# Kernel optimization log

Hardware: AMD Instinct MI355X
Metric: run time of the kernel (lower is better)

The kernel has to match this reference:

```python
import jax, jax.numpy as jnp
import numpy as np

MAXTIME = 1406073600
MINTIME = 832550400
SPAN = 10000
TIME_EMB = 100
N_GATE = 8
NUM_INTEREST = 4
DIM = 64
SEQ = 256
BATCH = 1024
ALPHA = 0.1
PI = 3.14159  # matches the literal in the source


def _build_time_table():
    # TimeEncoder: interleaved sin/cos positional table over time buckets.
    n = MAXTIME // SPAN + 3
    pos = np.arange(n, dtype=np.float64)[:, None]
    div = np.exp(np.arange(TIME_EMB // 2, dtype=np.float64) * -(np.log(10000.0) / TIME_EMB))[None, :]
    te = np.zeros((n, TIME_EMB), dtype=np.float32)
    te[:, 0::2] = np.sin(pos * div)
    te[:, 1::2] = np.cos(pos * div)
    return jnp.asarray(te)

_TIME_TABLE = _build_time_table()


def _time_encode(t):
    idx = (t / SPAN).astype(jnp.int32)
    return _TIME_TABLE[idx - jnp.min(idx)]


def setup_inputs() -> dict:
    key = jax.random.key(0)
    ks = jax.random.split(key, 11)
    B, S, D, NI, G = BATCH, SEQ, DIM, NUM_INTEREST, N_GATE
    item_his_emb = jax.random.normal(ks[0], (B, S, D), jnp.float32)
    item_eb = jax.random.normal(ks[1], (B, D), jnp.float32)
    # query times near maxtime, history times strictly earlier -> positive deltas
    t_batch = MAXTIME - 1e6 * jax.random.uniform(ks[2], (B,), jnp.float32)
    t_his = MINTIME + (MAXTIME - MINTIME - 1e6) * jax.random.uniform(ks[3], (B, S), jnp.float32)
    mask = (jax.random.uniform(ks[4], (B, S)) > 0.3).astype(jnp.float32)
    W1 = jax.random.normal(ks[5], (3 * TIME_EMB, 100), jnp.float32) / np.sqrt(3 * TIME_EMB)
    b1 = jnp.zeros((100,), jnp.float32)
    W2 = jax.random.normal(ks[6], (100, 1), jnp.float32) * 0.1
    b2 = jnp.zeros((1,), jnp.float32)
    phase = 100000.0 * jax.random.uniform(ks[7], (1, 1, G), jnp.float32)
    tao = 86400.0 * jnp.array([[[1, 2, 7, 14, 30, 60, 365, 730]]], jnp.float32)
    ratio = 0.3 * jax.random.uniform(ks[8], (1, 1, G), jnp.float32)
    gate_emb = jax.random.normal(ks[9], (1, D, G), jnp.float32)
    w_bilinear = jax.random.normal(ks[10], (S, NI * D, D), jnp.float32)
    return {"item_his_emb": item_his_emb, "item_eb": item_eb, "t_batch": t_batch,
            "t_his": t_his, "mask": mask, "W1": W1, "b1": b1, "W2": W2, "b2": b2,
            "phase": phase, "tao": tao, "ratio": ratio, "gate_emb": gate_emb,
            "w_bilinear": w_bilinear, "ta": 2}


def reference(item_his_emb, item_eb, t_batch, t_his, mask, W1, b1, W2, b2,
              phase, tao, ratio, gate_emb, w_bilinear, ta):
    B, S, D = item_his_emb.shape
    NI = NUM_INTEREST
    # --- time factor ---
    t_tiled = jnp.broadcast_to(t_batch[:, None], (B, S))
    time_feature = jnp.concatenate([_time_encode(t_tiled), _time_encode(t_his),
                                    _time_encode(t_tiled - t_his)], axis=2)  # [B,S,300]
    hidden1 = jax.nn.relu(time_feature @ W1 + b1)
    t_factor = jnp.transpose(jax.nn.sigmoid(hidden1 @ W2 + b2), (0, 2, 1))  # [B,1,S]
    # --- circadian gate factor ---
    phi = jnp.mod(t_his[:, :, None] - phase, tao) / tao  # [B,S,G]
    gate = jnp.where(phi < ratio, jnp.maximum(jnp.sin(PI * phi / ratio), 0.0), ALPHA * phi)
    gate_ratio = jax.nn.softmax(jnp.einsum('bsd,dg->bsg', item_his_emb, gate_emb[0]), axis=2) * gate
    g_factor = jnp.sum(gate_ratio, axis=2)[:, None, :]  # [B,1,S]
    reg1 = jnp.linalg.norm(t_factor)
    reg2 = jnp.linalg.norm(ratio) + jnp.linalg.norm(phase) / 100000.0
    # ta == 2 branch
    loss_reg = 0.1 * reg1 + 1.0 * reg2 + 1.0 / reg1 + 0.1 / reg2
    factor = jnp.broadcast_to(t_factor + g_factor, (B, NI, S))
    # --- bilinear_type == 2 projection ---
    item_emb_hat = jnp.einsum('skd,bsd->bsk', w_bilinear, item_his_emb)  # [B,S,NI*D]
    item_emb_hat = item_emb_hat.reshape(B, S, NI, D).transpose(0, 2, 1, 3)  # [B,NI,S,D]
    hat_iter = jax.lax.stop_gradient(item_emb_hat)
    # --- dynamic routing, 3 iterations ---
    cw = jnp.zeros((B, NI, S), item_his_emb.dtype)
    amask = mask[:, None, :]
    cap = None
    for i in range(3):
        sw = jax.nn.softmax(cw, axis=1)           # softmax over interests
        sw = jnp.where(amask == 0, 0.0, sw)
        src = hat_iter if i < 2 else item_emb_hat
        cap = jnp.einsum('bks,bksd->bkd', sw, src)  # [B,NI,D]
        n2 = jnp.sum(cap * cap, axis=-1, keepdims=True)
        cap = (n2 / (1.0 + n2) / jnp.sqrt(n2 + 1e-9)) * cap  # squash
        if i < 2:
            delta = jnp.einsum('bksd,bkd->bks', hat_iter, cap) * factor
            cw = cw + delta
    interest_capsule = cap  # [B,NI,D]
    # --- hard readout ---
    atten = jax.nn.softmax(jnp.einsum('bkd,bd->bk', interest_capsule, item_eb), axis=1)
    readout = interest_capsule[jnp.arange(B), jnp.argmax(atten, axis=1)]  # [B,D]
    return interest_capsule, readout, loss_reg
```

## Files before the change

### kernel.cpp

```cpp
#include <hip/hip_runtime.h>
#include <math.h>
#include <limits.h>

#define BB 1024
#define SS 256
#define DD 64
#define NI 4
#define NG 8
#define TE_N 100
#define PMAX 57420
#define PMAXP 57424
#define P0MAX 128
#define TPB 16

typedef _Float16 half8 __attribute__((ext_vector_type(8)));
typedef _Float16 half4 __attribute__((ext_vector_type(4)));
typedef float f32x4 __attribute__((ext_vector_type(4)));

#define OFF_FTHT  ((size_t)0)
#define OFF_FDFT  ((size_t)TE_N*PMAXP)
#define OFF_GTBP  (OFF_FDFT + (size_t)TE_N*PMAXP)
#define OFF_FAC   (OFF_GTBP + (size_t)TE_N*P0MAX)
#define OFF_SCAL  (OFF_FAC + (size_t)BB*SS)
#define OFF_REC   (OFF_SCAL + 160)
#define OFF_SREC  (OFF_REC + (size_t)BB*SS*2)
#define OFF_HAT   (OFF_SREC + (size_t)BB*SS*2)

__device__ inline float dpp_add_xor1(float x){
    int i = __builtin_bit_cast(int, x);
    int p = __builtin_amdgcn_update_dpp(i, i, 0xB1, 0xF, 0xF, true);
    return x + __builtin_bit_cast(float, p);
}
__device__ inline float dpp_add_xor2(float x){
    int i = __builtin_bit_cast(int, x);
    int p = __builtin_amdgcn_update_dpp(i, i, 0x4E, 0xF, 0xF, true);
    return x + __builtin_bit_cast(float, p);
}
__device__ inline float swz_add_xor16(float x){
    int i = __builtin_bit_cast(int, x);
    int p = __builtin_amdgcn_ds_swizzle(i, 0x401F);
    return x + __builtin_bit_cast(float, p);
}

__global__ void k_init(float* ws){
    int t = threadIdx.x;
    int* ib = (int*)(ws + OFF_SCAL);
    if (t == 0){
        ib[0] = INT_MAX; ib[1] = INT_MAX; ib[2] = INT_MAX;
        ws[OFF_SCAL + 4] = 0.0f;
    }
    if (t >= 8 && t < 136) ib[t] = 0;
}

__global__ void k_min(const float* __restrict__ tb, const float* __restrict__ th, float* ws){
    int gid = blockIdx.x * blockDim.x + threadIdx.x;
    int stride = gridDim.x * blockDim.x;
    int m0 = INT_MAX, m1 = INT_MAX, m2 = INT_MAX;
    for (int i = gid; i < BB*SS; i += stride){
        float t  = th[i];
        float t2 = tb[i >> 8];
        int i1 = (int)(t / 10000.0f);
        int i2 = (int)((t2 - t) / 10000.0f);
        m1 = min(m1, i1);
        m2 = min(m2, i2);
    }
    if (gid < BB) m0 = (int)(tb[gid] / 10000.0f);
    #pragma unroll
    for (int off = 1; off < 64; off <<= 1){
        m0 = min(m0, __shfl_xor(m0, off));
        m1 = min(m1, __shfl_xor(m1, off));
        m2 = min(m2, __shfl_xor(m2, off));
    }
    if ((threadIdx.x & 63) == 0){
        int* mi = (int*)(ws + OFF_SCAL);
        atomicMin(mi + 0, m0);
        atomicMin(mi + 1, m1);
        atomicMin(mi + 2, m2);
    }
}

__global__ void k_tables(const float* __restrict__ W1, float* ws){
    int pbase = blockIdx.x * TPB;
    int t = threadIdx.x;
    __shared__ float te[TPB][TE_N];
    for (int idx = t; idx < TPB*50; idx += 128){
        int pp = idx / 50, h = idx - pp*50;
        double div = exp((double)h * -0.09210340371976184);
        double a = (double)(pbase + pp) * div;
        te[pp][2*h]   = (float)sin(a);
        te[pp][2*h+1] = (float)cos(a);
    }
    __syncthreads();
    if (t < TE_N){
        float a1[TPB], a2[TPB];
        #pragma unroll
        for (int pp = 0; pp < TPB; pp++){ a1[pp] = 0.f; a2[pp] = 0.f; }
        for (int i = 0; i < TE_N; i++){
            float w1v = W1[(100+i)*100 + t];
            float w2v = W1[(200+i)*100 + t];
            #pragma unroll
            for (int pp = 0; pp < TPB; pp++){
                float v = te[pp][i];
                a1[pp] += v * w1v;
                a2[pp] += v * w2v;
            }
        }
        for (int pp = 0; pp < TPB; pp++){
            int p = pbase + pp;
            if (p < PMAX){
                ws[OFF_FTHT + (size_t)t*PMAXP + p] = a1[pp];
                ws[OFF_FDFT + (size_t)t*PMAXP + p] = a2[pp];
            }
        }
    }
}

__global__ void k_gtbP(const float* __restrict__ W1, const float* __restrict__ b1, float* ws){
    int p0 = blockIdx.x;
    int t = threadIdx.x;
    __shared__ float te[TE_N];
    if (t < TE_N/2){
        double div = exp((double)t * -0.09210340371976184);
        double a = (double)p0 * div;
        te[2*t]   = (float)sin(a);
        te[2*t+1] = (float)cos(a);
    }
    __syncthreads();
    if (t < TE_N){
        float a1 = b1[t];
        for (int i = 0; i < TE_N; i++) a1 += te[i] * W1[i*100 + t];
        ws[OFF_GTBP + (size_t)t*P0MAX + p0] = a1;
    }
}

__global__ void __launch_bounds__(256) k_hist(const float* __restrict__ tb,
                                              const float* __restrict__ th, float* ws){
    __shared__ int lh[64];
    int t = threadIdx.x;
    if (t < 64) lh[t] = 0;
    __syncthreads();
    int gid = blockIdx.x*256 + t;
    int b = gid >> 8;
    const int* mi = (const int*)(ws + OFF_SCAL);
    float thv = th[gid], tbv = tb[b];
    int p1 = (int)(thv / 10000.0f) - mi[1];
    int p2 = (int)((tbv - thv) / 10000.0f) - mi[2];
    int p0 = (int)(tbv / 10000.0f) - mi[0];
    p1 = min(max(p1, 0), PMAX-1);
    p2 = min(max(p2, 0), PMAX-1);
    p0 = min(max(p0, 0), P0MAX-1);
    ((uint2*)(ws + OFF_REC))[gid] =
        make_uint2((unsigned)p1 | ((unsigned)p2 << 16), (unsigned)gid | ((unsigned)p0 << 20));
    atomicAdd(&lh[p1 >> 10], 1);
    __syncthreads();
    if (t < 64 && lh[t]) atomicAdd((int*)(ws + OFF_SCAL) + 8 + t, lh[t]);
}

__global__ void k_scan(float* ws){
    if (threadIdx.x == 0){
        int* g   = (int*)(ws + OFF_SCAL) + 8;
        int* cur = (int*)(ws + OFF_SCAL) + 72;
        int acc = 0;
        for (int i = 0; i < 64; i++){ cur[i] = acc; acc += g[i]; }
    }
}

__global__ void __launch_bounds__(256) k_scatter(float* ws){
    __shared__ int lh[64], lbase[64];
    int t = threadIdx.x;
    if (t < 64) lh[t] = 0;
    __syncthreads();
    int gid = blockIdx.x*256 + t;
    uint2 r = ((const uint2*)(ws + OFF_REC))[gid];
    int bkt = (int)(r.x & 0xFFFFu) >> 10;
    int myloc = atomicAdd(&lh[bkt], 1);
    __syncthreads();
    if (t < 64 && lh[t]) lbase[t] = atomicAdd((int*)(ws + OFF_SCAL) + 72 + t, lh[t]);
    __syncthreads();
    ((uint2*)(ws + OFF_SREC))[lbase[bkt] + myloc] = r;
}

__global__ void __launch_bounds__(256) k_factor2(const float* __restrict__ W2,
                         const float* __restrict__ b2, float* ws){
    int t = threadIdx.x;
    int bid = blockIdx.x;
    int sbid = (bid & 7)*128 + (bid >> 3);
    int q = sbid*256 + t;
    uint2 r = ((const uint2*)(ws + OFF_SREC))[q];
    int p1  = (int)(r.x & 0xFFFFu);
    int p2  = (int)(r.x >> 16);
    int gid = (int)(r.y & 0xFFFFFu);
    int p0  = (int)(r.y >> 20);

    const float* ft = ws + OFF_FTHT + p1;
    const float* fd = ws + OFF_FDFT + p2;
    const float* gp = ws + OFF_GTBP + p0;

    float z = 0.f;
    #pragma unroll 10
    for (int j = 0; j < TE_N; j++){
        float a = ft[(size_t)j*PMAXP];
        float c = fd[(size_t)j*PMAXP];
        float g = gp[(size_t)j*P0MAX];
        z += fmaxf(g + a + c, 0.f) * W2[j];
    }
    float tf = 1.f / (1.f + expf(-(z + b2[0])));
    ws[OFF_FAC + gid] = tf;

    float r1 = tf * tf;
    #pragma unroll
    for (int off = 1; off < 64; off <<= 1) r1 += __shfl_xor(r1, off);
    if ((t & 63) == 0) atomicAdd(ws + OFF_SCAL + 4, r1);
}

__global__ void __launch_bounds__(256) k_gate(const float* __restrict__ X,
      const float* __restrict__ th_, const float* __restrict__ phase,
      const float* __restrict__ tao, const float* __restrict__ ratio,
      const float* __restrict__ ge, float* ws){
    __shared__ float sge[NG][DD];
    int t = threadIdx.x;
    for (int i = t; i < DD*NG; i += 256) sge[i & 7][i >> 3] = ge[i];
    __syncthreads();
    int gid = blockIdx.x * 256 + t;

    float lg[NG];
    #pragma unroll
    for (int g = 0; g < NG; g++) lg[g] = 0.f;
    const float4* xr = (const float4*)(X + (size_t)gid*DD);
    #pragma unroll 4
    for (int dc = 0; dc < 16; dc++){
        float4 xv = xr[dc];
        #pragma unroll
        for (int g = 0; g < NG; g++){
            lg[g] += xv.x*sge[g][dc*4+0] + xv.y*sge[g][dc*4+1]
                   + xv.z*sge[g][dc*4+2] + xv.w*sge[g][dc*4+3];
        }
    }
    float mx = lg[0];
    #pragma unroll
    for (int g = 1; g < NG; g++) mx = fmaxf(mx, lg[g]);
    float thv = th_[gid];
    float es = 0.f, gf = 0.f;
    #pragma unroll
    for (int g = 0; g < NG; g++){
        float e = expf(lg[g] - mx);
        es += e;
        float phv = fmodf(thv - phase[g], tao[g]) / tao[g];
        float gv = (phv < ratio[g]) ? fmaxf(sinf(3.14159f*phv/ratio[g]), 0.f) : 0.1f*phv;
        gf += e * gv;
    }
    ws[OFF_FAC + gid] += gf / es;
}

__global__ void __launch_bounds__(512, 2)
k_hat(const float* __restrict__ X, const float* __restrict__ Wb,
      float* __restrict__ hat, int b0, int nb){
    int btile = blockIdx.x;
    int s     = blockIdx.y;
    int t     = threadIdx.x;
    int rows = nb - btile*64; if (rows > 64) rows = 64;

    __shared__ _Float16 lds[40960];

    const float* xbase = X + ((size_t)(b0 + btile*64)*SS + s)*DD;
    #pragma unroll
    for (int i = 0; i < 2; i++){
        int q = t + 512*i;
        int r = q >> 4, jf = q & 15;
        float4 v;
        if (r < rows) v = *(const float4*)(xbase + (size_t)r*SS*DD + jf*4);
        else { v.x = 0.f; v.y = 0.f; v.z = 0.f; v.w = 0.f; }
        half4 h, l;
        h.x = (_Float16)v.x; h.y = (_Float16)v.y; h.z = (_Float16)v.z; h.w = (_Float16)v.w;
        l.x = (_Float16)(v.x - (float)h.x); l.y = (_Float16)(v.y - (float)h.y);
        l.z = (_Float16)(v.z - (float)h.z); l.w = (_Float16)(v.w - (float)h.w);
        int bt = r >> 4, rowin = r & 15;
        int j0 = jf*4;
        int kk = j0 >> 5, jb = (j0 & 31) >> 3, e0 = j0 & 7;
        int lane = rowin + 16*jb;
        int base = ((bt*2 + kk)*2)*512 + lane*8 + e0;
        *(half4*)(lds + base)       = h;
        *(half4*)(lds + base + 512) = l;
    }
    const float* wbase = Wb + (size_t)s*16384;
    #pragma unroll
    for (int i = 0; i < 8; i++){
        int q = t + 512*i;
        int kd = q >> 4, jf = q & 15;
        float4 v = *(const float4*)(wbase + kd*64 + jf*4);
        half4 h, l;
        h.x = (_Float16)v.x; h.y = (_Float16)v.y; h.z = (_Float16)v.z; h.w = (_Float16)v.w;
        l.x = (_Float16)(v.x - (float)h.x); l.y = (_Float16)(v.y - (float)h.y);
        l.z = (_Float16)(v.z - (float)h.z); l.w = (_Float16)(v.w - (float)h.w);
        int kdt = kd >> 4, rowin = kd & 15;
        int j0 = jf*4;
        int kk = j0 >> 5, jb = (j0 & 31) >> 3, e0 = j0 & 7;
        int lane = rowin + 16*jb;
        int base = 8192 + ((kdt*2 + kk)*2)*512 + lane*8 + e0;
        *(half4*)(lds + base)       = h;
        *(half4*)(lds + base + 512) = l;
    }
    __syncthreads();

    int w    = t >> 6;
    int lane = t & 63;
    int wbt  = w >> 1;
    int kdh  = w & 1;

    half8 a[2][2];
    #pragma unroll
    for (int kk = 0; kk < 2; kk++)
        #pragma unroll
        for (int hl = 0; hl < 2; hl++)
            a[kk][hl] = *(half8*)(lds + ((wbt*2 + kk)*2 + hl)*512 + lane*8);

    int brow = (lane >> 4) * 4;
    int bcol = lane & 15;

    #pragma unroll
    for (int kdti = 0; kdti < 8; kdti++){
        int kdt = kdh*8 + kdti;
        const _Float16* wb0 = lds + 8192 + ((kdt*2 + 0)*2)*512 + lane*8;
        const _Float16* wb1 = lds + 8192 + ((kdt*2 + 1)*2)*512 + lane*8;
        half8 bh0 = *(half8*)(wb0);
        half8 bl0 = *(half8*)(wb0 + 512);
        half8 bh1 = *(half8*)(wb1);
        half8 bl1 = *(half8*)(wb1 + 512);
        f32x4 acc = {0.f, 0.f, 0.f, 0.f};
        acc = __builtin_amdgcn_mfma_f32_16x16x32_f16(a[0][0], bh0, acc, 0, 0, 0);
        acc = __builtin_amdgcn_mfma_f32_16x16x32_f16(a[0][0], bl0, acc, 0, 0, 0);
        acc = __builtin_amdgcn_mfma_f32_16x16x32_f16(a[0][1], bh0, acc, 0, 0, 0);
        acc = __builtin_amdgcn_mfma_f32_16x16x32_f16(a[1][0], bh1, acc, 0, 0, 0);
        acc = __builtin_amdgcn_mfma_f32_16x16x32_f16(a[1][0], bl1, acc, 0, 0, 0);
        acc = __builtin_amdgcn_mfma_f32_16x16x32_f16(a[1][1], bh1, acc, 0, 0, 0);
        int kd = kdt*16 + bcol;
        #pragma unroll
        for (int r = 0; r < 4; r++){
            int rl = wbt*16 + brow + r;
            if (rl < rows)
                hat[((size_t)(btile*64 + rl)*SS + s)*256 + kd] = acc[r];
        }
    }
}

__global__ void __launch_bounds__(1024) k_route(const float* __restrict__ eb,
                                                const float* __restrict__ mask_,
                                                const float* __restrict__ ws,
                                                const float* __restrict__ hat,
                                                float* __restrict__ out, int b0){
    int bl = blockIdx.x;
    int b = b0 + bl;
    int t = threadIdx.x;
    int lane = t & 63, wv = t >> 6;
    int k = (lane >> 2) & 3;
    int s_local = (lane & 3) | (((lane >> 4) & 3) << 2);
    int s = wv * 16 + s_local;
    __shared__ float part[16][4][64];
    __shared__ float capl[4][68];
    __shared__ float logits[4];
    __shared__ int kms;

    float hat_r[64];
    const float4* hsrc = (const float4*)(hat + (size_t)bl*65536 + ((size_t)s*4 + k)*64);
    #pragma unroll
    for (int jc = 0; jc < 16; jc++){
        float4 v = hsrc[jc];
        hat_r[4*jc] = v.x; hat_r[4*jc+1] = v.y; hat_r[4*jc+2] = v.z; hat_r[4*jc+3] = v.w;
    }
    float fac = ws[OFF_FAC + (size_t)b*SS + s];
    float mk = mask_[(size_t)b*SS + s];
    float cw = 0.f;
    float capv = 0.f;

    for (int it = 0; it < 3; ++it){
        float sw;
        if (it == 0){
            sw = (mk == 0.f) ? 0.f : 0.25f;
        } else {
            float m = fmaxf(cw, __shfl_xor(cw, 4)); m = fmaxf(m, __shfl_xor(m, 8));
            float e = expf(cw - m);
            float ssum = e + __shfl_xor(e, 4); ssum += __shfl_xor(ssum, 8);
            sw = (mk == 0.f) ? 0.f : (e / ssum);
        }

        #pragma unroll
        for (int c = 0; c < 4; c++){
            float tmp[16];
            #pragma unroll
            for (int i = 0; i < 16; i++) tmp[i] = sw * hat_r[c*16 + i];
            #pragma unroll
            for (int i = 0; i < 16; i++) tmp[i] = dpp_add_xor1(tmp[i]);
            #pragma unroll
            for (int i = 0; i < 16; i++) tmp[i] = dpp_add_xor2(tmp[i]);
            #pragma unroll
            for (int i = 0; i < 16; i++) tmp[i] = swz_add_xor16(tmp[i]);
            #pragma unroll
            for (int i = 0; i < 16; i++) tmp[i] += __shfl_xor(tmp[i], 32);
            if ((lane & 0x33) == 0){
                float* dst = &part[wv][lane >> 2][c*16];
                #pragma unroll
                for (int i = 0; i < 4; i++)
                    ((float4*)dst)[i] = make_float4(tmp[4*i], tmp[4*i+1], tmp[4*i+2], tmp[4*i+3]);
            }
        }
        __syncthreads();
        if (t < 256){
            int k2 = t >> 6, d = t & 63;
            float cp = 0.f;
            #pragma unroll
            for (int w2 = 0; w2 < 16; w2++) cp += part[w2][k2][d];
            float q = cp * cp;
            #pragma unroll
            for (int msk = 1; msk < 64; msk <<= 1) q += __shfl_xor(q, msk);
            float sc = q / ((1.f + q) * sqrtf(q + 1e-9f));
            capv = sc * cp;
            capl[k2][d] = capv;
        }
        __syncthreads();
        if (it < 2){
            const float4* cp4 = (const float4*)&capl[k][0];
            float dot = 0.f;
            #pragma unroll
            for (int jc = 0; jc < 16; jc++){
                float4 v = cp4[jc];
                dot += hat_r[4*jc]*v.x + hat_r[4*jc+1]*v.y + hat_r[4*jc+2]*v.z + hat_r[4*jc+3]*v.w;
            }
            cw += dot * fac;
        }
        __syncthreads();
    }

    if (t < 256){
        int k2 = t >> 6, d = t & 63;
        out[(size_t)b*256 + t] = capv;
        float qq = capv * eb[(size_t)b*DD + d];
        #pragma unroll
        for (int msk = 1; msk < 64; msk <<= 1) qq += __shfl_xor(qq, msk);
        if (lane == 0) logits[k2] = qq;
    }
    __syncthreads();
    if (t == 0){
        float best = logits[0]; int km = 0;
        for (int kk = 1; kk < 4; kk++) if (logits[kk] > best){ best = logits[kk]; km = kk; }
        kms = km;
    }
    __syncthreads();
    if (t < 64) out[(size_t)BB*256 + (size_t)b*64 + t] = capl[kms][t];
}

__global__ void k_final(const float* __restrict__ phase, const float* __restrict__ ratio,
                        float* ws, float* __restrict__ out){
    if (threadIdx.x == 0){
        float r2a = 0.f, r2b = 0.f;
        for (int g = 0; g < NG; g++){ r2a += ratio[g]*ratio[g]; r2b += phase[g]*phase[g]; }
        float reg2 = sqrtf(r2a) + sqrtf(r2b) / 100000.0f;
        float reg1 = sqrtf(ws[OFF_SCAL + 4]);
        out[(size_t)BB*256 + (size_t)BB*64] = 0.1f*reg1 + reg2 + 1.0f/reg1 + 0.1f/reg2;
    }
}

extern "C" void kernel_launch(void* const* d_in, const int* in_sizes, int n_in,
                              void* d_out, int out_size, void* d_ws, size_t ws_size,
                              hipStream_t stream){
    const float* Xh = (const float*)d_in[0];
    const float* eb = (const float*)d_in[1];
    const float* tb = (const float*)d_in[2];
    const float* th = (const float*)d_in[3];
    const float* mk = (const float*)d_in[4];
    const float* W1 = (const float*)d_in[5];
    const float* b1 = (const float*)d_in[6];
    const float* W2 = (const float*)d_in[7];
    const float* b2 = (const float*)d_in[8];
    const float* ph = (const float*)d_in[9];
    const float* ta = (const float*)d_in[10];
    const float* ra = (const float*)d_in[11];
    const float* ge = (const float*)d_in[12];
    const float* wb = (const float*)d_in[13];
    float* out = (float*)d_out;
    float* ws  = (float*)d_ws;

    hipLaunchKernelGGL(k_init,    dim3(1),     dim3(256), 0, stream, ws);
    hipLaunchKernelGGL(k_min,     dim3(256),   dim3(256), 0, stream, tb, th, ws);
    hipLaunchKernelGGL(k_tables,  dim3((PMAX+TPB-1)/TPB), dim3(128), 0, stream, W1, ws);
    hipLaunchKernelGGL(k_gtbP,    dim3(P0MAX), dim3(128), 0, stream, W1, b1, ws);
    hipLaunchKernelGGL(k_hist,    dim3(BB),    dim3(256), 0, stream, tb, th, ws);
    hipLaunchKernelGGL(k_scan,    dim3(1),     dim3(64),  0, stream, ws);
    hipLaunchKernelGGL(k_scatter, dim3(BB),    dim3(256), 0, stream, ws);
    hipLaunchKernelGGL(k_factor2, dim3(BB),    dim3(256), 0, stream, W2, b2, ws);
    hipLaunchKernelGGL(k_gate,    dim3(BB),    dim3(256), 0, stream, Xh, th, ph, ta, ra, ge, ws);

    long wfloats  = (long)(ws_size / sizeof(float));
    long hatavail = wfloats - (long)OFF_HAT;
    int CH = (int)(hatavail / 65536);
    if (CH > BB) CH = BB;
    if (CH >= 128) CH &= ~127;
    if (CH < 1)  CH = 1;
    float* hatbuf = ws + OFF_HAT;
    for (int c0 = 0; c0 < BB; c0 += CH){
        int nb = BB - c0; if (nb > CH) nb = CH;
        int nbt = (nb + 63) / 64;
        hipLaunchKernelGGL(k_hat,   dim3(nbt, 256), dim3(512),  0, stream, Xh, wb, hatbuf, c0, nb);
        hipLaunchKernelGGL(k_route, dim3(nb),       dim3(1024), 0, stream, eb, mk, ws, hatbuf, out, c0);
    }
    hipLaunchKernelGGL(k_final, dim3(1), dim3(64), 0, stream, ph, ra, ws, out);
}
```

Before: 525.4 us.

## Split factor MLP hidden dim across blocks and rework table kernel tiling

The factor kernel now splits the 100 hidden units into four groups of 25 on a second grid dimension. Each group writes a partial pre-activation to a new workspace buffer, and a new k_fsig kernel sums the four partials, applies the sigmoid and does the regularisation reduction. The table kernel is re-tiled to 64 positions per 256-thread block, with one output column per wave taken via readfirstlane, which gives coalesced stores along p. The changes aim to raise parallelism and memory-level concurrency, at the cost of an extra launch and a 4×B×S float partial buffer that reduces the space left for the hat chunk.

Result: slower. 608.7 us (+15.9%).

```diff
diff --git a/kernel.cpp b/kernel.cpp
--- a/kernel.cpp
+++ b/kernel.cpp
@@ -11,7 +11,8 @@
 #define PMAX 57420
 #define PMAXP 57424
 #define P0MAX 128
-#define TPB 16
+#define TPB2 64
+#define NPAIR ((size_t)BB*SS)
 
 typedef _Float16 half8 __attribute__((ext_vector_type(8)));
 typedef _Float16 half4 __attribute__((ext_vector_type(4)));
@@ -23,8 +24,9 @@
 #define OFF_FAC   (OFF_GTBP + (size_t)TE_N*P0MAX)
 #define OFF_SCAL  (OFF_FAC + (size_t)BB*SS)
 #define OFF_REC   (OFF_SCAL + 160)
-#define OFF_SREC  (OFF_REC + (size_t)BB*SS*2)
-#define OFF_HAT   (OFF_SREC + (size_t)BB*SS*2)
+#define OFF_SREC  (OFF_REC + NPAIR*2)
+#define OFF_ZP    (OFF_SREC + NPAIR*2)
+#define OFF_HAT   (OFF_ZP + 4*NPAIR)
 
 __device__ inline float dpp_add_xor1(float x){
     int i = __builtin_bit_cast(int, x);
@@ -79,11 +81,11 @@
     }
 }
 
-__global__ void k_tables(const float* __restrict__ W1, float* ws){
-    int pbase = blockIdx.x * TPB;
-    int t = threadIdx.x;
-    __shared__ float te[TPB][TE_N];
-    for (int idx = t; idx < TPB*50; idx += 128){
+__global__ void __launch_bounds__(256) k_tables(const float* __restrict__ W1, float* ws){
+    int pbase = blockIdx.x * TPB2;
+    int t = threadIdx.x;
+    __shared__ float te[TPB2][102];
+    for (int idx = t; idx < TPB2*50; idx += 256){
         int pp = idx / 50, h = idx - pp*50;
         double div = exp((double)h * -0.09210340371976184);
         double a = (double)(pbase + pp) * div;
@@ -91,26 +93,21 @@
         te[pp][2*h+1] = (float)cos(a);
     }
     __syncthreads();
-    if (t < TE_N){
-        float a1[TPB], a2[TPB];
-        #pragma unroll
-        for (int pp = 0; pp < TPB; pp++){ a1[pp] = 0.f; a2[pp] = 0.f; }
+    #pragma unroll 5
+    for (int k = 0; k < 25; k++){
+        int o = t + 256*k;
+        int j = __builtin_amdgcn_readfirstlane(o >> 6);
+        int pp = o & 63;
+        int p = pbase + pp;
+        float a1 = 0.f, a2 = 0.f;
         for (int i = 0; i < TE_N; i++){
-            float w1v = W1[(100+i)*100 + t];
-            float w2v = W1[(200+i)*100 + t];
-            #pragma unroll
-            for (int pp = 0; pp < TPB; pp++){
-                float v = te[pp][i];
-                a1[pp] += v * w1v;
-                a2[pp] += v * w2v;
-            }
-        }
-        for (int pp = 0; pp < TPB; pp++){
-            int p = pbase + pp;
-            if (p < PMAX){
-                ws[OFF_FTHT + (size_t)t*PMAXP + p] = a1[pp];
-                ws[OFF_FDFT + (size_t)t*PMAXP + p] = a2[pp];
-            }
+            float v = te[pp][i];
+            a1 += v * W1[(100+i)*100 + j];
+            a2 += v * W1[(200+i)*100 + j];
+        }
+        if (p < PMAX){
+            ws[OFF_FTHT + (size_t)j*PMAXP + p] = a1;
+            ws[OFF_FDFT + (size_t)j*PMAXP + p] = a2;
         }
     }
 }
@@ -180,37 +177,45 @@
     ((uint2*)(ws + OFF_SREC))[lbase[bkt] + myloc] = r;
 }
 
-__global__ void __launch_bounds__(256) k_factor2(const float* __restrict__ W2,
-                         const float* __restrict__ b2, float* ws){
+__global__ void __launch_bounds__(256) k_factor2(const float* __restrict__ W2, float* ws){
     int t = threadIdx.x;
     int bid = blockIdx.x;
+    int jh  = blockIdx.y;
     int sbid = (bid & 7)*128 + (bid >> 3);
     int q = sbid*256 + t;
     uint2 r = ((const uint2*)(ws + OFF_SREC))[q];
     int p1  = (int)(r.x & 0xFFFFu);
     int p2  = (int)(r.x >> 16);
-    int gid = (int)(r.y & 0xFFFFFu);
     int p0  = (int)(r.y >> 20);
 
-    const float* ft = ws + OFF_FTHT + p1;
-    const float* fd = ws + OFF_FDFT + p2;
-    const float* gp = ws + OFF_GTBP + p0;
+    const float* ft = ws + OFF_FTHT + (size_t)(jh*25)*PMAXP + p1;
+    const float* fd = ws + OFF_FDFT + (size_t)(jh*25)*PMAXP + p2;
+    const float* gp = ws + OFF_GTBP + (size_t)(jh*25)*P0MAX + p0;
+    const float* w2 = W2 + jh*25;
 
     float z = 0.f;
-    #pragma unroll 10
-    for (int j = 0; j < TE_N; j++){
+    #pragma unroll
+    for (int j = 0; j < 25; j++){
         float a = ft[(size_t)j*PMAXP];
         float c = fd[(size_t)j*PMAXP];
         float g = gp[(size_t)j*P0MAX];
-        z += fmaxf(g + a + c, 0.f) * W2[j];
-    }
+        z += fmaxf(g + a + c, 0.f) * w2[j];
+    }
+    ws[OFF_ZP + (size_t)jh*NPAIR + q] = z;
+}
+
+__global__ void __launch_bounds__(256) k_fsig(const float* __restrict__ b2, float* ws){
+    int q = blockIdx.x*256 + threadIdx.x;
+    float z = (ws[OFF_ZP + q] + ws[OFF_ZP + NPAIR + q])
+            + (ws[OFF_ZP + 2*NPAIR + q] + ws[OFF_ZP + 3*NPAIR + q]);
+    unsigned ry = ((const uint2*)(ws + OFF_SREC))[q].y;
+    int gid = (int)(ry & 0xFFFFFu);
     float tf = 1.f / (1.f + expf(-(z + b2[0])));
     ws[OFF_FAC + gid] = tf;
-
     float r1 = tf * tf;
     #pragma unroll
     for (int off = 1; off < 64; off <<= 1) r1 += __shfl_xor(r1, off);
-    if ((t & 63) == 0) atomicAdd(ws + OFF_SCAL + 4, r1);
+    if ((threadIdx.x & 63) == 0) atomicAdd(ws + OFF_SCAL + 4, r1);
 }
 
 __global__ void __launch_bounds__(256) k_gate(const float* __restrict__ X,
@@ -481,12 +486,13 @@
 
     hipLaunchKernelGGL(k_init,    dim3(1),     dim3(256), 0, stream, ws);
     hipLaunchKernelGGL(k_min,     dim3(256),   dim3(256), 0, stream, tb, th, ws);
-    hipLaunchKernelGGL(k_tables,  dim3((PMAX+TPB-1)/TPB), dim3(128), 0, stream, W1, ws);
+    hipLaunchKernelGGL(k_tables,  dim3((PMAX+TPB2-1)/TPB2), dim3(256), 0, stream, W1, ws);
     hipLaunchKernelGGL(k_gtbP,    dim3(P0MAX), dim3(128), 0, stream, W1, b1, ws);
     hipLaunchKernelGGL(k_hist,    dim3(BB),    dim3(256), 0, stream, tb, th, ws);
     hipLaunchKernelGGL(k_scan,    dim3(1),     dim3(64),  0, stream, ws);
     hipLaunchKernelGGL(k_scatter, dim3(BB),    dim3(256), 0, stream, ws);
-    hipLaunchKernelGGL(k_factor2, dim3(BB),    dim3(256), 0, stream, W2, b2, ws);
+    hipLaunchKernelGGL(k_factor2, dim3(1024, 4), dim3(256), 0, stream, W2, ws);
+    hipLaunchKernelGGL(k_fsig,    dim3(1024),  dim3(256), 0, stream, b2, ws);
     hipLaunchKernelGGL(k_gate,    dim3(BB),    dim3(256), 0, stream, Xh, th, ph, ta, ra, ge, ws);
 
     long wfloats  = (long)(ws_size / sizeof(float));
```
